# Optimization experiments

Measured on AMD Instinct MI355X. Metric: run time of the kernel, lower is better.

## Reference

```python
import jax, jax.numpy as jnp
import numpy as np

B, T, D, H, C = 32, 2048, 256, 256, 128


def setup_inputs() -> dict:
    key = jax.random.key(0)
    ks = jax.random.split(key, 4)
    s = 0.05  # small init to avoid gate saturation
    return {
        "x": jax.random.normal(ks[0], (B, T, D), jnp.float32),
        "W_gate": jax.random.normal(ks[1], (D + H, 2 * H), jnp.float32) * s,
        "b_gate": jnp.ones((2 * H,), jnp.float32),  # TF GRUCell gate bias init = 1.0
        "W_cand": jax.random.normal(ks[2], (D + H, H), jnp.float32) * s,
        "b_cand": jnp.zeros((H,), jnp.float32),
        "W_proj": jax.random.normal(ks[3], (H, C), jnp.float32) * s,
        "b_proj": jnp.zeros((C,), jnp.float32),
    }


def reference(x, W_gate, b_gate, W_cand, b_cand, W_proj, b_proj):
    # Split the TF concat([x, h]) kernels into input and recurrent parts.
    Wx_g, Wh_g = W_gate[:D], W_gate[D:]
    Wx_c, Wh_c = W_cand[:D], W_cand[D:]
    # Batch the input-to-hidden GEMMs over all timesteps at once.
    gx = jnp.einsum('btd,dg->btg', x, Wx_g) + b_gate   # [B,T,2H]
    cx = jnp.einsum('btd,dh->bth', x, Wx_c) + b_cand   # [B,T,H]

    def step(h, inp):
        gxt, cxt = inp                                  # [B,2H], [B,H]
        gates = jax.nn.sigmoid(gxt + h @ Wh_g)          # r, u gates
        r, u = gates[:, :H], gates[:, H:]
        c = jnp.tanh(cxt + (r * h) @ Wh_c)              # candidate
        h_new = u * h + (1.0 - u) * c                   # TF GRUCell update
        return h_new, h_new

    h0 = jnp.zeros((x.shape[0], H), x.dtype)
    gx_t = jnp.swapaxes(gx, 0, 1)                       # time-major for scan
    cx_t = jnp.swapaxes(cx, 0, 1)
    _, ys = jax.lax.scan(step, h0, (gx_t, cx_t))        # [T,B,H]
    # Per-timestep linear + sigmoid projection (one batched GEMM).
    out = jax.nn.sigmoid(jnp.einsum('tbh,hc->tbc', ys, W_proj) + b_proj)
    return jnp.swapaxes(out, 0, 1)                      # [B,T,C]
```

## Files before the change

kernel.cpp:

```cpp
#include <hip/hip_runtime.h>
#include <cstdint>
#include <cstddef>

#define BB 32
#define TT 2048
#define DD 256
#define HH 256
#define CC 128
#define GG 512

#if defined(__has_builtin)
#  if __has_builtin(__builtin_amdgcn_fdot2_f32_bf16)
#    define HAVE_BF16_DOT2 1
#  endif
#endif
#ifndef HAVE_BF16_DOT2
#  define HAVE_BF16_DOT2 0
#endif

#if HAVE_BF16_DOT2
typedef __bf16 bf16x2_t __attribute__((ext_vector_type(2)));
#endif

__device__ __forceinline__ float bflo(uint32_t w) { return __uint_as_float(w << 16); }
__device__ __forceinline__ float bfhi(uint32_t w) { return __uint_as_float(w & 0xffff0000u); }

__device__ __forceinline__ float dot2bf(uint32_t w, uint32_t h, float acc) {
#if HAVE_BF16_DOT2
  return __builtin_amdgcn_fdot2_f32_bf16(__builtin_bit_cast(bf16x2_t, w),
                                         __builtin_bit_cast(bf16x2_t, h),
                                         acc, false);
#else
  acc = fmaf(bflo(w), bflo(h), acc);
  acc = fmaf(bfhi(w), bfhi(h), acc);
  return acc;
#endif
}

__device__ __forceinline__ uint16_t f2bf(float x) {
  uint32_t u = __float_as_uint(x);
  uint32_t r = (u + 0x7fffu + ((u >> 16) & 1u)) >> 16;
  return (uint16_t)r;
}

__device__ __forceinline__ uint32_t pkbf(float a, float b) {
  return (uint32_t)f2bf(a) | ((uint32_t)f2bf(b) << 16);
}

__device__ __forceinline__ float sigm(float x) { return 1.f / (1.f + __expf(-x)); }
__device__ __forceinline__ float tanh_f(float x) {
  float e = __expf(-2.f * fabsf(x));
  float t = (1.f - e) / (1.f + e);
  return copysignf(t, x);
}

__global__ void prep_kernel(const float* __restrict__ Wg, const float* __restrict__ bg,
                            const float* __restrict__ Wc, const float* __restrict__ bc,
                            const float* __restrict__ Wp,
                            float* __restrict__ Bm, float* __restrict__ bias,
                            uint32_t* __restrict__ Whg2, uint32_t* __restrict__ Whc2,
                            uint32_t* __restrict__ Wp2) {
  int i = blockIdx.x * 256 + threadIdx.x;
  if (i < 196608) {
    int k = i / 768, n = i % 768;
    Bm[i] = (n < GG) ? Wg[k * GG + n] : Wc[k * HH + (n - GG)];
    return;
  }
  int j = i - 196608;
  if (j < 768) {
    bias[j] = (j < GG) ? bg[j] : bc[j - GG];
    return;
  }
  int a = i - 197376;
  if (a < 65536) {
    int k2 = a >> 9, jj = a & 511;
    Whg2[a] = pkbf(Wg[(DD + 2 * k2) * GG + jj], Wg[(DD + 2 * k2 + 1) * GG + jj]);
    return;
  }
  int c2 = i - 262912;
  if (c2 < 32768) {
    int k2 = c2 >> 8, jj = c2 & 255;
    Whc2[c2] = pkbf(Wc[(DD + 2 * k2) * HH + jj], Wc[(DD + 2 * k2 + 1) * HH + jj]);
    return;
  }
  int p2 = i - 295680;
  if (p2 < 16384) {
    int k2 = p2 >> 7, jj = p2 & 127;
    Wp2[p2] = pkbf(Wp[(2 * k2) * CC + jj], Wp[(2 * k2 + 1) * CC + jj]);
  }
}

__global__ __launch_bounds__(256) void gemm_in(const float* __restrict__ A,
                                               const float* __restrict__ Bm,
                                               const float* __restrict__ bias,
                                               float* __restrict__ Cm) {
  __shared__ __align__(16) float As[16][65];
  __shared__ __align__(16) float Bs[16][64];
  const int tidx = threadIdx.x;
  const int tx = tidx & 15;
  const int ty = tidx >> 4;
  const int m0 = blockIdx.y * 64;
  const int n0 = blockIdx.x * 64;
  float acc[4][4] = {};

  for (int k0 = 0; k0 < DD; k0 += 16) {
    {
      int rr = tidx >> 2;
      int c = (tidx & 3) * 4;
      float4 av = *(const float4*)(A + (size_t)(m0 + rr) * DD + k0 + c);
      As[c + 0][rr] = av.x; As[c + 1][rr] = av.y; As[c + 2][rr] = av.z; As[c + 3][rr] = av.w;
    }
    {
      int rr = tidx >> 6;
      int cc = tidx & 63;
      #pragma unroll
      for (int i = 0; i < 4; i++)
        Bs[rr + i * 4][cc] = Bm[(size_t)(k0 + rr + i * 4) * 768 + n0 + cc];
    }
    __syncthreads();
    #pragma unroll
    for (int kk = 0; kk < 16; kk++) {
      float a[4], bb[4];
      #pragma unroll
      for (int i = 0; i < 4; i++) a[i] = As[kk][ty * 4 + i];
      #pragma unroll
      for (int jj = 0; jj < 4; jj++) bb[jj] = Bs[kk][tx * 4 + jj];
      #pragma unroll
      for (int i = 0; i < 4; i++)
        #pragma unroll
        for (int jj = 0; jj < 4; jj++)
          acc[i][jj] = fmaf(a[i], bb[jj], acc[i][jj]);
    }
    __syncthreads();
  }
  float4 bv = *(const float4*)&bias[n0 + tx * 4];
  #pragma unroll
  for (int i = 0; i < 4; i++) {
    int m = m0 + ty * 4 + i;
    float4 o;
    o.x = acc[i][0] + bv.x; o.y = acc[i][1] + bv.y;
    o.z = acc[i][2] + bv.z; o.w = acc[i][3] + bv.w;
    *(float4*)(Cm + (size_t)m * 768 + n0 + tx * 4) = o;
  }
}

__global__ __launch_bounds__(512) __attribute__((amdgpu_waves_per_eu(2, 2)))
void rnn_scan32(float* __restrict__ gxc,
                const uint32_t* __restrict__ Whg2,
                const uint32_t* __restrict__ Whc2) {
  __shared__ __align__(16) uint32_t s_h2[128];
  __shared__ __align__(16) uint32_t s_rh2[128];
  __shared__ __align__(16) float s_pc[2][256];
  __shared__ __align__(16) float s_u[256];
  __shared__ __align__(16) float s_hf[256];

  const int tid = threadIdx.x;
  const int b = blockIdx.x;
  const int jc = tid & 255, kh = tid >> 8;

  uint32_t wg[128];
  #pragma unroll
  for (int i = 0; i < 128; i++) wg[i] = Whg2[i * 512 + tid];
  uint32_t wc[64];
  #pragma unroll
  for (int i = 0; i < 64; i++) wc[i] = Whc2[(kh * 64 + i) * 256 + jc];

  if (tid < 128) s_h2[tid] = 0u;
  if (tid < 256) s_hf[tid] = 0.f;

  float* gx_b = gxc + (size_t)b * TT * 768;
  float gv = gx_b[tid];
  float cxv = (tid < 256) ? gx_b[GG + tid] : 0.f;

  __syncthreads();

  for (int t = 0; t < TT; t++) {
    const int tn = (t + 1 < TT) ? (t + 1) : (TT - 1);
    const float* gx_n = gx_b + (size_t)tn * 768;
    float gv_n = gx_n[tid];
    float cx_n = (tid < 256) ? gx_n[GG + tid] : 0.f;

    float acc = gv;
    #pragma unroll
    for (int k2 = 0; k2 < 128; k2 += 4) {
      uint4 hh = *(const uint4*)&s_h2[k2];
      acc = dot2bf(wg[k2 + 0], hh.x, acc);
      acc = dot2bf(wg[k2 + 1], hh.y, acc);
      acc = dot2bf(wg[k2 + 2], hh.z, acc);
      acc = dot2bf(wg[k2 + 3], hh.w, acc);
    }
    float g = sigm(acc);
    if (tid < 256) {
      ((uint16_t*)s_rh2)[tid] = f2bf(g * s_hf[tid]);
    } else {
      s_u[tid - 256] = g;
    }
    __syncthreads();

    {
      float ac = 0.f;
      #pragma unroll
      for (int i = 0; i < 64; i += 4) {
        uint4 rq = *(const uint4*)&s_rh2[kh * 64 + i];
        ac = dot2bf(wc[i + 0], rq.x, ac);
        ac = dot2bf(wc[i + 1], rq.y, ac);
        ac = dot2bf(wc[i + 2], rq.z, ac);
        ac = dot2bf(wc[i + 3], rq.w, ac);
      }
      s_pc[kh][jc] = ac;
    }
    __syncthreads();

    if (tid < 256) {
      float pre = cxv + s_pc[0][tid] + s_pc[1][tid];
      float c = tanh_f(pre);
      float u = s_u[tid];
      float hf = s_hf[tid];
      float hn = u * hf + (1.f - u) * c;
      s_hf[tid] = hn;
      uint16_t hb = f2bf(hn);
      ((uint16_t*)s_h2)[tid] = hb;
      ((uint16_t*)(gx_b + (size_t)t * 768 + GG))[tid] = hb;
    }
    __syncthreads();

    gv = gv_n; cxv = cx_n;
  }
}

__global__ __launch_bounds__(512) void proj_out(const uint32_t* __restrict__ gxcu,
                                                const uint32_t* __restrict__ Wp2,
                                                const float* __restrict__ bp,
                                                float* __restrict__ out) {
  __shared__ uint32_t s_wpT[16384];
  const int tid = threadIdx.x;

  #pragma unroll
  for (int i = 0; i < 8; i++) {
    int q = tid + i * 512;
    uint4 v = ((const uint4*)Wp2)[q];
    int k2 = q >> 5;
    int c0 = (q & 31) * 4;
    s_wpT[(c0 + 0) * 128 + (k2 ^ (((c0 + 0) & 7) << 2))] = v.x;
    s_wpT[(c0 + 1) * 128 + (k2 ^ (((c0 + 1) & 7) << 2))] = v.y;
    s_wpT[(c0 + 2) * 128 + (k2 ^ (((c0 + 2) & 7) << 2))] = v.z;
    s_wpT[(c0 + 3) * 128 + (k2 ^ (((c0 + 3) & 7) << 2))] = v.w;
  }
  __syncthreads();

  const int col = tid & 127;
  const int rsub = tid >> 7;
  const float bpc = bp[col];
  const int base = blockIdx.x * 256;
  const int cswz = (col & 7) << 2;

  for (int rr = 0; rr < 64; rr++) {
    int m = base + rr * 4 + rsub;
    const uint32_t* hrow = gxcu + (size_t)m * 768 + 512;
    float acc = bpc;
    #pragma unroll 8
    for (int i2 = 0; i2 < 32; i2++) {
      uint4 hq = *(const uint4*)&hrow[4 * i2];
      uint4 wq = *(const uint4*)&s_wpT[col * 128 + ((4 * i2) ^ cswz)];
      acc = dot2bf(wq.x, hq.x, acc);
      acc = dot2bf(wq.y, hq.y, acc);
      acc = dot2bf(wq.z, hq.z, acc);
      acc = dot2bf(wq.w, hq.w, acc);
    }
    out[(size_t)m * 128 + col] = sigm(acc);
  }
}

extern "C" void kernel_launch(void* const* d_in, const int* in_sizes, int n_in,
                              void* d_out, int out_size, void* d_ws, size_t ws_size,
                              hipStream_t stream) {
  const float* x  = (const float*)d_in[0];
  const float* Wg = (const float*)d_in[1];
  const float* bg = (const float*)d_in[2];
  const float* Wc = (const float*)d_in[3];
  const float* bc = (const float*)d_in[4];
  const float* Wp = (const float*)d_in[5];
  const float* bp = (const float*)d_in[6];
  float* out = (float*)d_out;

  char* w = (char*)d_ws;
  float*    gxc  = (float*)   (w);
  float*    Bm   = (float*)   (w + 201326592ull);
  float*    bias = (float*)   (w + 202113024ull);
  uint32_t* Whg2 = (uint32_t*)(w + 202116096ull);
  uint32_t* Whc2 = (uint32_t*)(w + 202378240ull);
  uint32_t* Wp2  = (uint32_t*)(w + 202509312ull);

  prep_kernel<<<1219, 256, 0, stream>>>(Wg, bg, Wc, bc, Wp, Bm, bias, Whg2, Whc2, Wp2);
  gemm_in<<<dim3(12, 1024), 256, 0, stream>>>(x, Bm, bias, gxc);
  rnn_scan32<<<BB, 512, 0, stream>>>(gxc, Whg2, Whc2);
  proj_out<<<256, 512, 0, stream>>>((const uint32_t*)gxc, Wp2, bp, out);
}
```

Baseline: 3.720 ms.

## Split recurrent dot products into 4-output x K-slice thread tiles with shared reductions

The per-step recurrent matvecs are re-partitioned. Each thread now computes four adjacent outputs over a slice of K: 4 K-groups for the gate matvec and 8 for the candidate. Partial sums go to shared memory and are reduced afterwards. Each LDS load of h is reused across four accumulators, which cuts shared-memory read traffic and breaks the serial dependency chain, at the cost of an extra barrier per timestep and more LDS writes for the partial sums.

```diff
diff --git a/kernel.cpp b/kernel.cpp
--- a/kernel.cpp
+++ b/kernel.cpp
@@ -145,25 +145,37 @@
 }
 
 __global__ __launch_bounds__(512) __attribute__((amdgpu_waves_per_eu(2, 2)))
-void rnn_scan32(float* __restrict__ gxc,
-                const uint32_t* __restrict__ Whg2,
-                const uint32_t* __restrict__ Whc2) {
+void rnn_scan32b(float* __restrict__ gxc,
+                 const uint32_t* __restrict__ Whg2,
+                 const uint32_t* __restrict__ Whc2) {
   __shared__ __align__(16) uint32_t s_h2[128];
   __shared__ __align__(16) uint32_t s_rh2[128];
-  __shared__ __align__(16) float s_pc[2][256];
+  __shared__ __align__(16) float s_pg[4][512];
+  __shared__ __align__(16) float s_pc[8][256];
   __shared__ __align__(16) float s_u[256];
   __shared__ __align__(16) float s_hf[256];
 
   const int tid = threadIdx.x;
   const int b = blockIdx.x;
-  const int jc = tid & 255, kh = tid >> 8;
+  const int jg = tid & 127;
+  const int kg = tid >> 7;
+  const int jc = tid & 63;
+  const int kc = tid >> 6;
 
   uint32_t wg[128];
   #pragma unroll
-  for (int i = 0; i < 128; i++) wg[i] = Whg2[i * 512 + tid];
+  for (int i = 0; i < 32; i++) {
+    #pragma unroll
+    for (int c = 0; c < 4; c++)
+      wg[4 * i + c] = Whg2[(32 * kg + i) * 512 + 4 * jg + c];
+  }
   uint32_t wc[64];
   #pragma unroll
-  for (int i = 0; i < 64; i++) wc[i] = Whc2[(kh * 64 + i) * 256 + jc];
+  for (int i = 0; i < 16; i++) {
+    #pragma unroll
+    for (int c = 0; c < 4; c++)
+      wc[4 * i + c] = Whc2[(16 * kc + i) * 256 + 4 * jc + c];
+  }
 
   if (tid < 128) s_h2[tid] = 0u;
   if (tid < 256) s_hf[tid] = 0.f;
@@ -180,39 +192,75 @@
     float gv_n = gx_n[tid];
     float cx_n = (tid < 256) ? gx_n[GG + tid] : 0.f;
 
-    float acc = gv;
-    #pragma unroll
-    for (int k2 = 0; k2 < 128; k2 += 4) {
-      uint4 hh = *(const uint4*)&s_h2[k2];
-      acc = dot2bf(wg[k2 + 0], hh.x, acc);
-      acc = dot2bf(wg[k2 + 1], hh.y, acc);
-      acc = dot2bf(wg[k2 + 2], hh.z, acc);
-      acc = dot2bf(wg[k2 + 3], hh.w, acc);
-    }
-    float g = sigm(acc);
+    {
+      float a0 = 0.f, a1 = 0.f, a2 = 0.f, a3 = 0.f;
+      #pragma unroll
+      for (int i4 = 0; i4 < 8; i4++) {
+        uint4 hh = *(const uint4*)&s_h2[32 * kg + 4 * i4];
+        a0 = dot2bf(wg[16 * i4 + 0], hh.x, a0);
+        a1 = dot2bf(wg[16 * i4 + 1], hh.x, a1);
+        a2 = dot2bf(wg[16 * i4 + 2], hh.x, a2);
+        a3 = dot2bf(wg[16 * i4 + 3], hh.x, a3);
+        a0 = dot2bf(wg[16 * i4 + 4], hh.y, a0);
+        a1 = dot2bf(wg[16 * i4 + 5], hh.y, a1);
+        a2 = dot2bf(wg[16 * i4 + 6], hh.y, a2);
+        a3 = dot2bf(wg[16 * i4 + 7], hh.y, a3);
+        a0 = dot2bf(wg[16 * i4 + 8], hh.z, a0);
+        a1 = dot2bf(wg[16 * i4 + 9], hh.z, a1);
+        a2 = dot2bf(wg[16 * i4 + 10], hh.z, a2);
+        a3 = dot2bf(wg[16 * i4 + 11], hh.z, a3);
+        a0 = dot2bf(wg[16 * i4 + 12], hh.w, a0);
+        a1 = dot2bf(wg[16 * i4 + 13], hh.w, a1);
+        a2 = dot2bf(wg[16 * i4 + 14], hh.w, a2);
+        a3 = dot2bf(wg[16 * i4 + 15], hh.w, a3);
+      }
+      float4 pv; pv.x = a0; pv.y = a1; pv.z = a2; pv.w = a3;
+      *(float4*)&s_pg[kg][4 * jg] = pv;
+    }
+    __syncthreads();
+
+    {
+      float acc = gv + s_pg[0][tid] + s_pg[1][tid] + s_pg[2][tid] + s_pg[3][tid];
+      float g = sigm(acc);
+      if (tid < 256) {
+        ((uint16_t*)s_rh2)[tid] = f2bf(g * s_hf[tid]);
+      } else {
+        s_u[tid - 256] = g;
+      }
+    }
+    __syncthreads();
+
+    {
+      float a0 = 0.f, a1 = 0.f, a2 = 0.f, a3 = 0.f;
+      #pragma unroll
+      for (int i4 = 0; i4 < 4; i4++) {
+        uint4 rq = *(const uint4*)&s_rh2[16 * kc + 4 * i4];
+        a0 = dot2bf(wc[16 * i4 + 0], rq.x, a0);
+        a1 = dot2bf(wc[16 * i4 + 1], rq.x, a1);
+        a2 = dot2bf(wc[16 * i4 + 2], rq.x, a2);
+        a3 = dot2bf(wc[16 * i4 + 3], rq.x, a3);
+        a0 = dot2bf(wc[16 * i4 + 4], rq.y, a0);
+        a1 = dot2bf(wc[16 * i4 + 5], rq.y, a1);
+        a2 = dot2bf(wc[16 * i4 + 6], rq.y, a2);
+        a3 = dot2bf(wc[16 * i4 + 7], rq.y, a3);
+        a0 = dot2bf(wc[16 * i4 + 8], rq.z, a0);
+        a1 = dot2bf(wc[16 * i4 + 9], rq.z, a1);
+        a2 = dot2bf(wc[16 * i4 + 10], rq.z, a2);
+        a3 = dot2bf(wc[16 * i4 + 11], rq.z, a3);
+        a0 = dot2bf(wc[16 * i4 + 12], rq.w, a0);
+        a1 = dot2bf(wc[16 * i4 + 13], rq.w, a1);
+        a2 = dot2bf(wc[16 * i4 + 14], rq.w, a2);
+        a3 = dot2bf(wc[16 * i4 + 15], rq.w, a3);
+      }
+      float4 pv; pv.x = a0; pv.y = a1; pv.z = a2; pv.w = a3;
+      *(float4*)&s_pc[kc][4 * jc] = pv;
+    }
+    __syncthreads();
+
     if (tid < 256) {
-      ((uint16_t*)s_rh2)[tid] = f2bf(g * s_hf[tid]);
-    } else {
-      s_u[tid - 256] = g;
-    }
-    __syncthreads();
-
-    {
-      float ac = 0.f;
-      #pragma unroll
-      for (int i = 0; i < 64; i += 4) {
-        uint4 rq = *(const uint4*)&s_rh2[kh * 64 + i];
-        ac = dot2bf(wc[i + 0], rq.x, ac);
-        ac = dot2bf(wc[i + 1], rq.y, ac);
-        ac = dot2bf(wc[i + 2], rq.z, ac);
-        ac = dot2bf(wc[i + 3], rq.w, ac);
-      }
-      s_pc[kh][jc] = ac;
-    }
-    __syncthreads();
-
-    if (tid < 256) {
-      float pre = cxv + s_pc[0][tid] + s_pc[1][tid];
+      float pre = cxv;
+      #pragma unroll
+      for (int k = 0; k < 8; k++) pre += s_pc[k][tid];
       float c = tanh_f(pre);
       float u = s_u[tid];
       float hf = s_hf[tid];
@@ -293,6 +341,6 @@
 
   prep_kernel<<<1219, 256, 0, stream>>>(Wg, bg, Wc, bc, Wp, Bm, bias, Whg2, Whc2, Wp2);
   gemm_in<<<dim3(12, 1024), 256, 0, stream>>>(x, Bm, bias, gxc);
-  rnn_scan32<<<BB, 512, 0, stream>>>(gxc, Whg2, Whc2);
+  rnn_scan32b<<<BB, 512, 0, stream>>>(gxc, Whg2, Whc2);
   proj_out<<<256, 512, 0, stream>>>((const uint32_t*)gxc, Wp2, bp, out);
 }
```

After: 3.306 ms. -11.1%, faster.
